# Kernel tuning notes

Measured on AMD Instinct MI355X. Metric: run time of the kernel, lower is better.

Reference implementation:

```python
import jax, jax.numpy as jnp
import numpy as np

N_HASHES = 4
CHUNK = 144
REDUCTION = 4
RES_SCALE = 1.0
NORM_EPS = 5e-5


def conv2d(x, w, b, pad):
    y = jax.lax.conv_general_dilated(
        x, w, window_strides=(1, 1), padding=[(pad, pad), (pad, pad)],
        dimension_numbers=('NCHW', 'OIHW', 'NCHW'))
    return y + b[None, :, None, None]


def add_adjacent_buckets(x):
    # x: (N, h, n_chunks, chunk, e); concat each chunk with its circular neighbors
    back = jnp.roll(x, 1, axis=2)
    fwd = jnp.roll(x, -1, axis=2)
    return jnp.concatenate([x, back, fwd], axis=3)


def setup_inputs() -> dict:
    key = jax.random.key(0)
    ks = jax.random.split(key, 6)
    x = jax.random.normal(ks[0], (1, 32, 192, 192), jnp.float32)
    w_match = jax.random.normal(ks[1], (8, 32, 3, 3), jnp.float32) * 0.05
    b_match = jnp.zeros((8,), jnp.float32)
    w_asm = jax.random.normal(ks[2], (32, 32, 1, 1), jnp.float32) * 0.05
    b_asm = jnp.zeros((32,), jnp.float32)
    rotations = jax.random.normal(ks[3], (8, N_HASHES, 64), jnp.float32)
    return {'x': x, 'w_match': w_match, 'b_match': b_match,
            'w_asm': w_asm, 'b_asm': b_asm, 'rotations': rotations}


def reference(x, w_match, b_match, w_asm, b_asm, rotations):
    N, _, H, W = x.shape
    L = H * W
    # conv_match: 3x3 conv 32->8; conv_assembly: 1x1 conv 32->32
    x_embed = conv2d(x, w_match, b_match, 1).reshape(N, -1, L).transpose(0, 2, 1)  # (N, L, 8)
    y_embed = conv2d(x, w_asm, b_asm, 0).reshape(N, -1, L).transpose(0, 2, 1)      # (N, L, 32)
    C = x_embed.shape[-1]
    hash_buckets = min(L // CHUNK + (L // CHUNK) % 2, 128)  # = 128 here

    # --- LSH hashing (non-differentiable; rotations passed in for determinism) ---
    rotated = jnp.einsum('blf,fhi->bhli', x_embed, rotations)        # (N, h, L, hb/2)
    rotated = jnp.concatenate([rotated, -rotated], axis=-1)          # (N, h, L, hb)
    hash_codes = jnp.argmax(rotated, axis=-1)                        # (N, h, L)
    hash_codes = hash_codes + (jnp.arange(N_HASHES) * hash_buckets)[None, :, None]
    hash_codes = hash_codes.reshape(N, -1)                           # (N, h*L)

    # --- sort tokens by bucket id ---
    indices = jnp.argsort(hash_codes, axis=-1)
    undo_sort = jnp.argsort(indices, axis=-1)
    mod_indices = indices % L
    x_sorted = jnp.take_along_axis(x_embed, mod_indices[:, :, None], axis=1)  # (N, h*L, 8)
    y_sorted = jnp.take_along_axis(y_embed, mod_indices[:, :, None], axis=1)  # (N, h*L, 32)

    x_b = x_sorted.reshape(N, N_HASHES, -1, C)
    y_b = y_sorted.reshape(N, N_HASHES, -1, C * REDUCTION)
    padding = (-L) % CHUNK  # static; 0 for L=192*192
    if padding:
        x_b = jnp.concatenate([x_b, x_b[:, :, -padding:, :]], axis=2)
        y_b = jnp.concatenate([y_b, y_b[:, :, -padding:, :]], axis=2)
    x_b = x_b.reshape(N, N_HASHES, -1, CHUNK, C)
    y_b = y_b.reshape(N, N_HASHES, -1, CHUNK, C * REDUCTION)

    # --- bucketed attention with adjacent buckets ---
    nrm = jnp.linalg.norm(x_b, axis=-1, keepdims=True)
    x_match = x_b / jnp.maximum(nrm, NORM_EPS)   # F.normalize(eps=5e-5)
    x_match = add_adjacent_buckets(x_match)      # (N, h, k, 3*chunk, 8)
    y_adj = add_adjacent_buckets(y_b)            # (N, h, k, 3*chunk, 32)

    raw = jnp.einsum('bhkie,bhkje->bhkij', x_b, x_match)  # (N, h, k, 144, 432)
    bucket_score = jax.scipy.special.logsumexp(raw, axis=-1, keepdims=True)
    score = jnp.exp(raw - bucket_score)
    ret = jnp.einsum('bhkij,bhkje->bhkie', score, y_adj)  # (N, h, k, 144, 32)

    ret = ret.reshape(N, N_HASHES, -1, C * REDUCTION)
    bucket_score = bucket_score.reshape(N, N_HASHES, -1)
    if padding:
        ret = ret[:, :, :-padding, :]
        bucket_score = bucket_score[:, :, :-padding]
    ret = ret.reshape(N, -1, C * REDUCTION)
    bucket_score = bucket_score.reshape(N, -1)

    # --- unsort and combine hash rounds via softmax over logsumexp scores ---
    ret = jnp.take_along_axis(ret, undo_sort[:, :, None], axis=1)
    bucket_score = jnp.take_along_axis(bucket_score, undo_sort, axis=1)
    ret = ret.reshape(N, N_HASHES, L, C * REDUCTION)
    probs = jax.nn.softmax(bucket_score.reshape(N, N_HASHES, L, 1), axis=1)
    out = jnp.sum(ret * probs, axis=1)                     # (N, L, 32)
    out = out.transpose(0, 2, 1).reshape(N, -1, H, W) * RES_SCALE + x
    return out
```

## Files before the change

### kernel.cpp

```cpp
#include <hip/hip_runtime.h>
#include <hip/hip_bf16.h>
#include <math.h>

#define LTOT 36864
#define NH 4
#define NCHUNK 256
#define CHU 144
#define NBUCK 128
#define NSEG 144
#define HW_ 192
#define VTS 148

typedef unsigned int u32;
typedef unsigned short u16;
typedef unsigned long long u64;
typedef __attribute__((ext_vector_type(4))) short short4v;
typedef __attribute__((ext_vector_type(4))) float f32x4;

__device__ __forceinline__ u32 pkbf(float a, float b){
  union { __hip_bfloat162 h2; u32 u; } cv;
  cv.h2 = __float22bfloat162_rn(float2{a,b});
  return cv.u;
}
__device__ __forceinline__ float bflo(u32 w){ return __uint_as_float(w<<16); }
__device__ __forceinline__ float bfhi(u32 w){ return __uint_as_float(w & 0xffff0000u); }

__global__ __launch_bounds__(256) void k_conv(const float* __restrict__ x,
    const float* __restrict__ wm, const float* __restrict__ bm,
    const float* __restrict__ wa, const float* __restrict__ ba,
    const float* __restrict__ rot,
    float* __restrict__ xe, u16* __restrict__ Vu, int* __restrict__ code)
{
  __shared__ float xs[32*108];
  __shared__ float xq[64*8];
  const int t = threadIdx.x;
  const int id = blockIdx.x;
  const int bx = id % 12, by = id / 12;

  for (int idx=t; idx<3456; idx+=256){
    int ci = idx/108, rem = idx-ci*108;
    int iy = rem/18,  ix = rem-iy*18;
    int yy = by*4+iy-1, xx = bx*16+ix-1;
    float v = 0.f;
    if (yy>=0 && yy<HW_ && xx>=0 && xx<HW_) v = x[ci*LTOT + yy*HW_ + xx];
    xs[idx] = v;
  }
  __syncthreads();
  const int lane = t & 63;
  const int w  = __builtin_amdgcn_readfirstlane(t>>6);
  const int co0 = 2*w, cb = 8*w;
  const int ix = lane & 15, iy = lane >> 4;
  float a0 = bm[co0], a1 = bm[co0+1];
  float acc[8];
  #pragma unroll
  for (int co=0;co<8;co++) acc[co] = ba[cb+co];
  const float* xb  = xs + iy*18 + ix;
  const float* w0p = wm + co0*288;
  const float* w1p = w0p + 288;
  for (int ci=0; ci<32; ci++){
    const float* xp = xb + ci*108;
    float x00=xp[0],  x01=xp[1],  x02=xp[2];
    float x10=xp[18], x11=xp[19], x12=xp[20];
    float x20=xp[36], x21=xp[37], x22=xp[38];
    const float* w0 = w0p + ci*9;
    const float* w1 = w1p + ci*9;
    a0 += x00*w0[0]+x01*w0[1]+x02*w0[2]
        + x10*w0[3]+x11*w0[4]+x12*w0[5]
        + x20*w0[6]+x21*w0[7]+x22*w0[8];
    a1 += x00*w1[0]+x01*w1[1]+x02*w1[2]
        + x10*w1[3]+x11*w1[4]+x12*w1[5]
        + x20*w1[6]+x21*w1[7]+x22*w1[8];
    const float* wap = wa + cb*32 + ci;
    #pragma unroll
    for (int co=0;co<8;co++) acc[co] += x11 * wap[co*32];
  }
  const int l = (by*4+iy)*HW_ + bx*16+ix;
  *(float2*)(xe + l*8 + co0) = float2{a0,a1};
  *(float2*)(xq + lane*8 + co0) = float2{a0,a1};
  uint4 vv;
  vv.x = pkbf(acc[0],acc[1]); vv.y = pkbf(acc[2],acc[3]);
  vv.z = pkbf(acc[4],acc[5]); vv.w = pkbf(acc[6],acc[7]);
  *(uint4*)(Vu + (size_t)l*32 + cb) = vv;
  __syncthreads();

  const int h = w;
  const float4* qp = (const float4*)(xq + lane*8);
  float4 qa = qp[0], qb = qp[1];
  float best = -INFINITY; int bi = 0;
  float worst = INFINITY; int wi = 0;
  for (int i=0; i<64; i++){
    const float* rp = rot + h*64 + i;
    float v = qa.x*rp[0]    + qa.y*rp[256]  + qa.z*rp[512]  + qa.w*rp[768]
            + qb.x*rp[1024] + qb.y*rp[1280] + qb.z*rp[1536] + qb.w*rp[1792];
    if (v > best)  { best  = v; bi = i; }
    if (v < worst) { worst = v; wi = i; }
  }
  int c = (-worst > best) ? (64+wi) : bi;
  const int ly = lane >> 4, lx = lane & 15;
  code[h*LTOT + (by*4+ly)*HW_ + bx*16+lx] = c;
}

__global__ __launch_bounds__(256) void k_rank(const int* __restrict__ code,
    int* __restrict__ lrank, int* __restrict__ hist)
{
  const int h = blockIdx.y, seg = blockIdx.x, t = threadIdx.x;
  const int l = seg*256 + t;
  int c = code[h*LTOT + l];

  const int lane = t & 63, w = t >> 6;
  u64 mask = ~0ull;
  #pragma unroll
  for (int bit=0; bit<7; bit++){
    u64 bset = __ballot((c>>bit)&1);
    mask &= ((c>>bit)&1) ? bset : ~bset;
  }
  int rin = __popcll(mask & ((lane==0)?0ull:(~0ull >> (64-lane))));
  int cnt = __popcll(mask);

  __shared__ int wh[4][NBUCK];
  ((int*)wh)[t] = 0; ((int*)wh)[t+256] = 0;
  __syncthreads();
  if (rin == 0) wh[w][c] = cnt;
  __syncthreads();
  int r = rin;
  for (int ww=0; ww<w; ww++) r += wh[ww][c];
  lrank[h*LTOT + l] = r;
  if (t < NBUCK) hist[(h*NSEG+seg)*NBUCK + t] = wh[0][t]+wh[1][t]+wh[2][t]+wh[3][t];
}

__global__ __launch_bounds__(512) void k_scan(const int* __restrict__ hist,
    int* __restrict__ segoff)
{
  const int h = blockIdx.x;
  const int b = threadIdx.x & 127, g = threadIdx.x >> 7;
  int vals[36];
  int sum = 0;
  #pragma unroll
  for (int i=0;i<36;i++){
    vals[i] = hist[(h*NSEG + g*36 + i)*NBUCK + b];
    sum += vals[i];
  }
  __shared__ int ps[4][NBUCK];
  __shared__ int tot[NBUCK];
  __shared__ int scv[NBUCK];
  ps[g][b] = sum;
  __syncthreads();
  if (g == 0){
    int run = 0;
    #pragma unroll
    for (int gg=0; gg<4; gg++){ int tv = ps[gg][b]; ps[gg][b] = run; run += tv; }
    tot[b] = run;
    int v = run;
    #pragma unroll
    for (int off=1; off<64; off<<=1){
      int u = __shfl_up(v, off);
      if ((b & 63) >= off) v += u;
    }
    scv[b] = v;
  }
  __syncthreads();
  int base = scv[b] - tot[b] + ((b >= 64) ? scv[63] : 0);
  int run2 = base + ps[g][b];
  #pragma unroll
  for (int i=0;i<36;i++){
    segoff[(h*NSEG + g*36 + i)*NBUCK + b] = run2;
    run2 += vals[i];
  }
}

__global__ __launch_bounds__(256) void k_scatter(const int* __restrict__ code,
    const int* __restrict__ lrank, const int* __restrict__ segoff,
    const float* __restrict__ xe, const u16* __restrict__ Vu,
    int* __restrict__ spos, u16* __restrict__ Ks, u16* __restrict__ Qs,
    u16* __restrict__ Vs)
{
  const int h = blockIdx.y, seg = blockIdx.x, t = threadIdx.x;
  const int l = seg*256 + t;
  int c = code[h*LTOT + l];
  int r = segoff[(h*NSEG+seg)*NBUCK + c] + lrank[h*LTOT + l];
  spos[h*LTOT + r] = l;

  const float4* xr = (const float4*)(xe + l*8);
  float4 a = xr[0], b = xr[1];
  float n2 = a.x*a.x+a.y*a.y+a.z*a.z+a.w*a.w
           + b.x*b.x+b.y*b.y+b.z*b.z+b.w*b.w;
  float sc = 1.0f / fmaxf(sqrtf(n2), 5e-5f);
  uint4 kk, qq;
  kk.x = pkbf(a.x*sc,a.y*sc); kk.y = pkbf(a.z*sc,a.w*sc);
  kk.z = pkbf(b.x*sc,b.y*sc); kk.w = pkbf(b.z*sc,b.w*sc);
  qq.x = pkbf(a.x,a.y); qq.y = pkbf(a.z,a.w);
  qq.z = pkbf(b.x,b.y); qq.w = pkbf(b.z,b.w);
  *(uint4*)(Ks + (size_t)(h*LTOT + r)*8) = kk;
  *(uint4*)(Qs + (size_t)(h*LTOT + r)*8) = qq;

  const uint4* vr = (const uint4*)(Vu + (size_t)l*32);
  uint4* vp = (uint4*)(Vs + (size_t)(h*LTOT + r)*32);
  vp[0] = vr[0]; vp[1] = vr[1]; vp[2] = vr[2]; vp[3] = vr[3];
}

__global__ __launch_bounds__(320) void k_attn(const u16* __restrict__ Ks,
    const u16* __restrict__ Qs, const u16* __restrict__ Vs,
    const int* __restrict__ spos, u16* __restrict__ ret_u, float* __restrict__ bs_u)
{
  __shared__ __align__(16) u16 Klds[432*8];
  __shared__ __align__(16) u16 Qlds[CHU*8];
  __shared__ __align__(16) u16 VT[3][32*VTS];
  __shared__ float qn[CHU];
  __shared__ int spos_l[CHU];

  const int t = threadIdx.x;
  const int k = blockIdx.x, h = blockIdx.y;

  if (t < CHU){
    uint4 qv = *(const uint4*)(Qs + (size_t)(h*LTOT + k*CHU + t)*8);
    *(uint4*)(Qlds + t*8) = qv;
    float f0=bflo(qv.x), f1=bfhi(qv.x), f2=bflo(qv.y), f3=bfhi(qv.y);
    float f4=bflo(qv.z), f5=bfhi(qv.z), f6=bflo(qv.w), f7=bfhi(qv.w);
    qn[t] = sqrtf(f0*f0+f1*f1+f2*f2+f3*f3+f4*f4+f5*f5+f6*f6+f7*f7)*1.01f + 1e-6f;
    spos_l[t] = spos[h*LTOT + k*CHU + t];
    #pragma unroll
    for (int rr=0; rr<3; rr++){
      const int gkb = ((k + NCHUNK-1 + rr) & (NCHUNK-1)) * CHU;
      *(uint4*)(Klds + (rr*CHU + t)*8) =
          *(const uint4*)(Ks + (size_t)(h*LTOT + gkb + t)*8);
    }
  }
  for (int j = t; j < 432; j += 320){
    int p = j >> 1, hf = j & 1;
    int g = 2*p;
    int rg = g / CHU, lk = g - rg*CHU;
    const int gkb = ((k + NCHUNK-1 + rg) & (NCHUNK-1)) * CHU;
    const uint4* ra = (const uint4*)(Vs + (size_t)(h*LTOT + gkb + lk)*32);
    const uint4* rb = (const uint4*)(Vs + (size_t)(h*LTOT + gkb + lk+1)*32);
    uint4 A0 = ra[hf*2], A1 = ra[hf*2+1];
    uint4 B0 = rb[hf*2], B1 = rb[hf*2+1];
    u32 aw[8] = {A0.x,A0.y,A0.z,A0.w,A1.x,A1.y,A1.z,A1.w};
    u32 bw[8] = {B0.x,B0.y,B0.z,B0.w,B1.x,B1.y,B1.z,B1.w};
    int ebase = hf*16;
    u16* vtb = (u16*)VT[rg];
    #pragma unroll
    for (int m=0;m<8;m++){
      u32 al = aw[m]&0xffffu, ah = aw[m]>>16;
      u32 bl = bw[m]&0xffffu, bh = bw[m]>>16;
      *(u32*)&vtb[(ebase+2*m  )*VTS + lk] = al | (bl<<16);
      *(u32*)&vtb[(ebase+2*m+1)*VTS + lk] = ah | (bh<<16);
    }
  }
  __syncthreads();

  const int lane = t & 63;
  const int wv = t >> 6;
  const int q = lane & 15;
  const int quad = lane >> 4;
  const bool two = (wv < 4);
  const int tl0 = 2*wv;
  const int tl1 = two ? (2*wv+1) : 8;

  const short4v zs = {0,0,0,0};
  short4v bq0 = zs, bq1 = zs;
  if (quad < 2){
    bq0 = *(const short4v*)(Qlds + (tl0*16+q)*8 + quad*4);
    if (two) bq1 = *(const short4v*)(Qlds + (tl1*16+q)*8 + quad*4);
  }
  const float m0 = qn[tl0*16+q];
  const float m1 = two ? qn[tl1*16+q] : 0.f;

  f32x4 o00={0,0,0,0}, o01={0,0,0,0}, o10={0,0,0,0}, o11={0,0,0,0};
  float s0 = 0.f, s1 = 0.f;

  #pragma unroll 3
  for (int kt=0; kt<27; kt++){
    const int rg = kt / 9, ktl = kt - rg*9;
    const u16* vtb = VT[rg];
    short4v av = zs;
    if (quad < 2) av = *(const short4v*)(Klds + (kt*16+q)*8 + quad*4);
    f32x4 zc = {0.f,0.f,0.f,0.f};
    f32x4 stA = __builtin_amdgcn_mfma_f32_16x16x16bf16_1k(av, bq0, zc, 0,0,0);

    float pA0 = __expf(stA[0]-m0), pA1 = __expf(stA[1]-m0);
    float pA2 = __expf(stA[2]-m0), pA3 = __expf(stA[3]-m0);
    s0 += (pA0+pA1)+(pA2+pA3);
    union { u32 u[2]; short4v s4; } pkA;
    pkA.u[0] = pkbf(pA0,pA1); pkA.u[1] = pkbf(pA2,pA3);

    short4v va0 = *(const short4v*)(&vtb[ q    *VTS + ktl*16 + quad*4]);
    short4v va1 = *(const short4v*)(&vtb[(q+16)*VTS + ktl*16 + quad*4]);
    o00 = __builtin_amdgcn_mfma_f32_16x16x16bf16_1k(va0, pkA.s4, o00, 0,0,0);
    o01 = __builtin_amdgcn_mfma_f32_16x16x16bf16_1k(va1, pkA.s4, o01, 0,0,0);

    if (two){
      f32x4 stB = __builtin_amdgcn_mfma_f32_16x16x16bf16_1k(av, bq1, zc, 0,0,0);
      float pB0 = __expf(stB[0]-m1), pB1 = __expf(stB[1]-m1);
      float pB2 = __expf(stB[2]-m1), pB3 = __expf(stB[3]-m1);
      s1 += (pB0+pB1)+(pB2+pB3);
      union { u32 u[2]; short4v s4; } pkB;
      pkB.u[0] = pkbf(pB0,pB1); pkB.u[1] = pkbf(pB2,pB3);
      o10 = __builtin_amdgcn_mfma_f32_16x16x16bf16_1k(va0, pkB.s4, o10, 0,0,0);
      o11 = __builtin_amdgcn_mfma_f32_16x16x16bf16_1k(va1, pkB.s4, o11, 0,0,0);
    }
  }

  float st0 = s0;
  st0 += __shfl_xor(st0, 16); st0 += __shfl_xor(st0, 32);
  float inv0 = 1.0f/st0;

  const int pos0 = spos_l[tl0*16 + q];
  u16* rp0 = ret_u + (size_t)(h*LTOT + pos0)*32;
  uint2 wA, wB;
  wA.x = pkbf(o00[0]*inv0, o00[1]*inv0); wA.y = pkbf(o00[2]*inv0, o00[3]*inv0);
  wB.x = pkbf(o01[0]*inv0, o01[1]*inv0); wB.y = pkbf(o01[2]*inv0, o01[3]*inv0);
  *(uint2*)&rp0[quad*4]    = wA;
  *(uint2*)&rp0[16+quad*4] = wB;
  if (quad == 0) bs_u[h*LTOT + pos0] = m0 + __logf(st0);

  if (two){
    float st1 = s1;
    st1 += __shfl_xor(st1, 16); st1 += __shfl_xor(st1, 32);
    float inv1 = 1.0f/st1;
    const int pos1 = spos_l[tl1*16 + q];
    u16* rp1 = ret_u + (size_t)(h*LTOT + pos1)*32;
    wA.x = pkbf(o10[0]*inv1, o10[1]*inv1); wA.y = pkbf(o10[2]*inv1, o10[3]*inv1);
    wB.x = pkbf(o11[0]*inv1, o11[1]*inv1); wB.y = pkbf(o11[2]*inv1, o11[3]*inv1);
    *(uint2*)&rp1[quad*4]    = wA;
    *(uint2*)&rp1[16+quad*4] = wB;
    if (quad == 0) bs_u[h*LTOT + pos1] = m1 + __logf(st1);
  }
}

__global__ __launch_bounds__(256) void k_final(const float* __restrict__ x,
    const u16* __restrict__ ret_u, const float* __restrict__ bs_u,
    float* __restrict__ out)
{
  const int l  = blockIdx.x*64 + (threadIdx.x & 63);
  const int eg = threadIdx.x >> 6;
  float bs[NH];
  #pragma unroll
  for (int h=0;h<NH;h++) bs[h] = bs_u[h*LTOT + l];
  float m = fmaxf(fmaxf(bs[0],bs[1]), fmaxf(bs[2],bs[3]));
  float p[NH]; float s = 0.f;
  #pragma unroll
  for (int h=0;h<NH;h++){ p[h] = __expf(bs[h]-m); s += p[h]; }
  float inv = 1.0f/s;
  float o[8];
  #pragma unroll
  for (int e=0;e<8;e++) o[e]=0.f;
  #pragma unroll
  for (int h=0;h<NH;h++){
    float w = p[h]*inv;
    uint4 v = *(const uint4*)(ret_u + (size_t)(h*LTOT + l)*32 + eg*8);
    o[0] += w*bflo(v.x); o[1] += w*bfhi(v.x);
    o[2] += w*bflo(v.y); o[3] += w*bfhi(v.y);
    o[4] += w*bflo(v.z); o[5] += w*bfhi(v.z);
    o[6] += w*bflo(v.w); o[7] += w*bfhi(v.w);
  }
  #pragma unroll
  for (int e=0;e<8;e++){
    int ge = eg*8 + e;
    out[ge*LTOT + l] = o[e] + x[ge*LTOT + l];
  }
}

extern "C" void kernel_launch(void* const* d_in, const int* in_sizes, int n_in,
                              void* d_out, int out_size, void* d_ws, size_t ws_size,
                              hipStream_t stream)
{
  const float* x   = (const float*)d_in[0];
  const float* wm  = (const float*)d_in[1];
  const float* bm  = (const float*)d_in[2];
  const float* wa  = (const float*)d_in[3];
  const float* ba  = (const float*)d_in[4];
  const float* rot = (const float*)d_in[5];
  float* out = (float*)d_out;

  char* ws = (char*)d_ws;
  size_t off = 0;
  auto alloc = [&](size_t bytes)->void*{
    void* p = ws + off;
    off = (off + bytes + 255) & ~(size_t)255;
    return p;
  };
  float* xe     = (float*)alloc((size_t)LTOT*8*4);
  u16*   Vu     = (u16*)  alloc((size_t)LTOT*32*2);
  int*   code   = (int*)  alloc((size_t)NH*LTOT*4);
  int*   lrank  = (int*)  alloc((size_t)NH*LTOT*4);
  int*   hist   = (int*)  alloc((size_t)NH*NSEG*NBUCK*4);
  int*   segoff = (int*)  alloc((size_t)NH*NSEG*NBUCK*4);
  int*   spos   = (int*)  alloc((size_t)NH*LTOT*4);
  u16*   Ks     = (u16*)  alloc((size_t)NH*LTOT*8*2);
  u16*   Qs     = (u16*)  alloc((size_t)NH*LTOT*8*2);
  u16*   Vs     = (u16*)  alloc((size_t)NH*LTOT*32*2);
  u16*   ret_u  = (u16*)  alloc((size_t)NH*LTOT*32*2);
  float* bs_u   = (float*)alloc((size_t)NH*LTOT*4);

  hipLaunchKernelGGL(k_conv,    dim3(576),        dim3(256), 0, stream, x, wm, bm, wa, ba, rot, xe, Vu, code);
  hipLaunchKernelGGL(k_rank,    dim3(NSEG,NH),    dim3(256), 0, stream, code, lrank, hist);
  hipLaunchKernelGGL(k_scan,    dim3(NH),         dim3(512), 0, stream, hist, segoff);
  hipLaunchKernelGGL(k_scatter, dim3(NSEG,NH),    dim3(256), 0, stream, code, lrank, segoff, xe, Vu, spos, Ks, Qs, Vs);
  hipLaunchKernelGGL(k_attn,    dim3(NCHUNK,NH),  dim3(320), 0, stream, Ks, Qs, Vs, spos, ret_u, bs_u);
  hipLaunchKernelGGL(k_final,   dim3(576),        dim3(256), 0, stream, x, ret_u, bs_u, out);
}
```

Before: 130.3 us.

## Fuse histogram into conv and rank/scan into scatter, dropping two launches

The conv kernel now runs 512 threads per block, with one match channel and four assembly channels per wave instead of two and eight. It also builds the per-segment bucket histogram with global atomics after hashing. The separate rank and scan kernels are gone: each scatter block recomputes its intra-segment rank with ballots and its global offset by summing the histogram over all segments. This removes two launches and the lrank/segoff buffers, but adds a memset, atomics, and redundant prefix reads of 144 segments in every scatter block.

```diff
diff --git a/kernel.cpp b/kernel.cpp
--- a/kernel.cpp
+++ b/kernel.cpp
@@ -25,11 +25,12 @@
 __device__ __forceinline__ float bflo(u32 w){ return __uint_as_float(w<<16); }
 __device__ __forceinline__ float bfhi(u32 w){ return __uint_as_float(w & 0xffff0000u); }
 
-__global__ __launch_bounds__(256) void k_conv(const float* __restrict__ x,
+__global__ __launch_bounds__(512) void k_conv(const float* __restrict__ x,
     const float* __restrict__ wm, const float* __restrict__ bm,
     const float* __restrict__ wa, const float* __restrict__ ba,
     const float* __restrict__ rot,
-    float* __restrict__ xe, u16* __restrict__ Vu, int* __restrict__ code)
+    float* __restrict__ xe, u16* __restrict__ Vu, int* __restrict__ code,
+    int* __restrict__ hist)
 {
   __shared__ float xs[32*108];
   __shared__ float xq[64*8];
@@ -37,7 +38,7 @@
   const int id = blockIdx.x;
   const int bx = id % 12, by = id / 12;
 
-  for (int idx=t; idx<3456; idx+=256){
+  for (int idx=t; idx<3456; idx+=512){
     int ci = idx/108, rem = idx-ci*108;
     int iy = rem/18,  ix = rem-iy*18;
     int yy = by*4+iy-1, xx = bx*16+ix-1;
@@ -48,65 +49,83 @@
   __syncthreads();
   const int lane = t & 63;
   const int w  = __builtin_amdgcn_readfirstlane(t>>6);
-  const int co0 = 2*w, cb = 8*w;
+  const int co = w;
+  const int cb = 4*w;
   const int ix = lane & 15, iy = lane >> 4;
-  float a0 = bm[co0], a1 = bm[co0+1];
-  float acc[8];
-  #pragma unroll
-  for (int co=0;co<8;co++) acc[co] = ba[cb+co];
+  float a0 = bm[co];
+  float acc[4];
+  #pragma unroll
+  for (int j=0;j<4;j++) acc[j] = ba[cb+j];
   const float* xb  = xs + iy*18 + ix;
-  const float* w0p = wm + co0*288;
-  const float* w1p = w0p + 288;
+  const float* w0p = wm + co*288;
   for (int ci=0; ci<32; ci++){
     const float* xp = xb + ci*108;
     float x00=xp[0],  x01=xp[1],  x02=xp[2];
     float x10=xp[18], x11=xp[19], x12=xp[20];
     float x20=xp[36], x21=xp[37], x22=xp[38];
     const float* w0 = w0p + ci*9;
-    const float* w1 = w1p + ci*9;
     a0 += x00*w0[0]+x01*w0[1]+x02*w0[2]
         + x10*w0[3]+x11*w0[4]+x12*w0[5]
         + x20*w0[6]+x21*w0[7]+x22*w0[8];
-    a1 += x00*w1[0]+x01*w1[1]+x02*w1[2]
-        + x10*w1[3]+x11*w1[4]+x12*w1[5]
-        + x20*w1[6]+x21*w1[7]+x22*w1[8];
     const float* wap = wa + cb*32 + ci;
     #pragma unroll
-    for (int co=0;co<8;co++) acc[co] += x11 * wap[co*32];
+    for (int j=0;j<4;j++) acc[j] += x11 * wap[j*32];
   }
   const int l = (by*4+iy)*HW_ + bx*16+ix;
-  *(float2*)(xe + l*8 + co0) = float2{a0,a1};
-  *(float2*)(xq + lane*8 + co0) = float2{a0,a1};
-  uint4 vv;
+  xe[l*8 + co] = a0;
+  xq[lane*8 + co] = a0;
+  uint2 vv;
   vv.x = pkbf(acc[0],acc[1]); vv.y = pkbf(acc[2],acc[3]);
-  vv.z = pkbf(acc[4],acc[5]); vv.w = pkbf(acc[6],acc[7]);
-  *(uint4*)(Vu + (size_t)l*32 + cb) = vv;
-  __syncthreads();
-
-  const int h = w;
-  const float4* qp = (const float4*)(xq + lane*8);
-  float4 qa = qp[0], qb = qp[1];
-  float best = -INFINITY; int bi = 0;
-  float worst = INFINITY; int wi = 0;
-  for (int i=0; i<64; i++){
-    const float* rp = rot + h*64 + i;
-    float v = qa.x*rp[0]    + qa.y*rp[256]  + qa.z*rp[512]  + qa.w*rp[768]
-            + qb.x*rp[1024] + qb.y*rp[1280] + qb.z*rp[1536] + qb.w*rp[1792];
-    if (v > best)  { best  = v; bi = i; }
-    if (v < worst) { worst = v; wi = i; }
-  }
-  int c = (-worst > best) ? (64+wi) : bi;
-  const int ly = lane >> 4, lx = lane & 15;
-  code[h*LTOT + (by*4+ly)*HW_ + bx*16+lx] = c;
-}
-
-__global__ __launch_bounds__(256) void k_rank(const int* __restrict__ code,
-    int* __restrict__ lrank, int* __restrict__ hist)
+  *(uint2*)(Vu + (size_t)l*32 + cb) = vv;
+  __syncthreads();
+
+  if (t < 256){
+    const int h = w;
+    const float4* qp = (const float4*)(xq + lane*8);
+    float4 qa = qp[0], qb = qp[1];
+    float best = -INFINITY; int bi = 0;
+    float worst = INFINITY; int wi = 0;
+    for (int i=0; i<64; i++){
+      const float* rp = rot + h*64 + i;
+      float v = qa.x*rp[0]    + qa.y*rp[256]  + qa.z*rp[512]  + qa.w*rp[768]
+              + qb.x*rp[1024] + qb.y*rp[1280] + qb.z*rp[1536] + qb.w*rp[1792];
+      if (v > best)  { best  = v; bi = i; }
+      if (v < worst) { worst = v; wi = i; }
+    }
+    int c = (-worst > best) ? (64+wi) : bi;
+    const int ly = lane >> 4, lx = lane & 15;
+    const int lpix = (by*4+ly)*HW_ + bx*16+lx;
+    code[h*LTOT + lpix] = c;
+    atomicAdd(&hist[(h*NSEG + (lpix>>8))*NBUCK + c], 1);
+  }
+}
+
+__global__ __launch_bounds__(256) void k_scatter(const int* __restrict__ code,
+    const int* __restrict__ hist,
+    const float* __restrict__ xe, const u16* __restrict__ Vu,
+    int* __restrict__ spos, u16* __restrict__ Ks, u16* __restrict__ Qs,
+    u16* __restrict__ Vs)
 {
   const int h = blockIdx.y, seg = blockIdx.x, t = threadIdx.x;
   const int l = seg*256 + t;
   int c = code[h*LTOT + l];
 
+  __shared__ int pre2[2][NBUCK], tot2[2][NBUCK];
+  __shared__ int scv[NBUCK];
+  __shared__ int segbase[NBUCK];
+  __shared__ int wh[4][NBUCK];
+
+  {
+    const int b = t & 127, gg = t >> 7;
+    int pre = 0, tt = 0;
+    const int sA = gg*72;
+    for (int s = sA; s < sA+72; s++){
+      int v = hist[(h*NSEG+s)*NBUCK + b];
+      tt += v;
+      if (s < seg) pre += v;
+    }
+    pre2[gg][b] = pre; tot2[gg][b] = tt;
+  }
   const int lane = t & 63, w = t >> 6;
   u64 mask = ~0ull;
   #pragma unroll
@@ -116,68 +135,31 @@
   }
   int rin = __popcll(mask & ((lane==0)?0ull:(~0ull >> (64-lane))));
   int cnt = __popcll(mask);
-
-  __shared__ int wh[4][NBUCK];
   ((int*)wh)[t] = 0; ((int*)wh)[t+256] = 0;
   __syncthreads();
+
   if (rin == 0) wh[w][c] = cnt;
-  __syncthreads();
-  int r = rin;
-  for (int ww=0; ww<w; ww++) r += wh[ww][c];
-  lrank[h*LTOT + l] = r;
-  if (t < NBUCK) hist[(h*NSEG+seg)*NBUCK + t] = wh[0][t]+wh[1][t]+wh[2][t]+wh[3][t];
-}
-
-__global__ __launch_bounds__(512) void k_scan(const int* __restrict__ hist,
-    int* __restrict__ segoff)
-{
-  const int h = blockIdx.x;
-  const int b = threadIdx.x & 127, g = threadIdx.x >> 7;
-  int vals[36];
-  int sum = 0;
-  #pragma unroll
-  for (int i=0;i<36;i++){
-    vals[i] = hist[(h*NSEG + g*36 + i)*NBUCK + b];
-    sum += vals[i];
-  }
-  __shared__ int ps[4][NBUCK];
-  __shared__ int tot[NBUCK];
-  __shared__ int scv[NBUCK];
-  ps[g][b] = sum;
-  __syncthreads();
-  if (g == 0){
-    int run = 0;
-    #pragma unroll
-    for (int gg=0; gg<4; gg++){ int tv = ps[gg][b]; ps[gg][b] = run; run += tv; }
-    tot[b] = run;
-    int v = run;
+  if (t < NBUCK){
+    int tt = tot2[0][t] + tot2[1][t];
+    int v = tt;
     #pragma unroll
     for (int off=1; off<64; off<<=1){
       int u = __shfl_up(v, off);
-      if ((b & 63) >= off) v += u;
-    }
-    scv[b] = v;
-  }
-  __syncthreads();
-  int base = scv[b] - tot[b] + ((b >= 64) ? scv[63] : 0);
-  int run2 = base + ps[g][b];
-  #pragma unroll
-  for (int i=0;i<36;i++){
-    segoff[(h*NSEG + g*36 + i)*NBUCK + b] = run2;
-    run2 += vals[i];
-  }
-}
-
-__global__ __launch_bounds__(256) void k_scatter(const int* __restrict__ code,
-    const int* __restrict__ lrank, const int* __restrict__ segoff,
-    const float* __restrict__ xe, const u16* __restrict__ Vu,
-    int* __restrict__ spos, u16* __restrict__ Ks, u16* __restrict__ Qs,
-    u16* __restrict__ Vs)
-{
-  const int h = blockIdx.y, seg = blockIdx.x, t = threadIdx.x;
-  const int l = seg*256 + t;
-  int c = code[h*LTOT + l];
-  int r = segoff[(h*NSEG+seg)*NBUCK + c] + lrank[h*LTOT + l];
+      if ((t & 63) >= off) v += u;
+    }
+    scv[t] = v;
+  }
+  __syncthreads();
+
+  if (t < NBUCK){
+    int tt = tot2[0][t] + tot2[1][t];
+    int excl = scv[t] - tt + ((t >= 64) ? scv[63] : 0);
+    segbase[t] = excl + pre2[0][t] + pre2[1][t];
+  }
+  __syncthreads();
+
+  int r = segbase[c] + rin;
+  for (int ww=0; ww<w; ww++) r += wh[ww][c];
   spos[h*LTOT + r] = l;
 
   const float4* xr = (const float4*)(xe + l*8);
@@ -382,9 +364,7 @@
   float* xe     = (float*)alloc((size_t)LTOT*8*4);
   u16*   Vu     = (u16*)  alloc((size_t)LTOT*32*2);
   int*   code   = (int*)  alloc((size_t)NH*LTOT*4);
-  int*   lrank  = (int*)  alloc((size_t)NH*LTOT*4);
   int*   hist   = (int*)  alloc((size_t)NH*NSEG*NBUCK*4);
-  int*   segoff = (int*)  alloc((size_t)NH*NSEG*NBUCK*4);
   int*   spos   = (int*)  alloc((size_t)NH*LTOT*4);
   u16*   Ks     = (u16*)  alloc((size_t)NH*LTOT*8*2);
   u16*   Qs     = (u16*)  alloc((size_t)NH*LTOT*8*2);
@@ -392,10 +372,9 @@
   u16*   ret_u  = (u16*)  alloc((size_t)NH*LTOT*32*2);
   float* bs_u   = (float*)alloc((size_t)NH*LTOT*4);
 
-  hipLaunchKernelGGL(k_conv,    dim3(576),        dim3(256), 0, stream, x, wm, bm, wa, ba, rot, xe, Vu, code);
-  hipLaunchKernelGGL(k_rank,    dim3(NSEG,NH),    dim3(256), 0, stream, code, lrank, hist);
-  hipLaunchKernelGGL(k_scan,    dim3(NH),         dim3(512), 0, stream, hist, segoff);
-  hipLaunchKernelGGL(k_scatter, dim3(NSEG,NH),    dim3(256), 0, stream, code, lrank, segoff, xe, Vu, spos, Ks, Qs, Vs);
+  hipMemsetAsync(hist, 0, (size_t)NH*NSEG*NBUCK*4, stream);
+  hipLaunchKernelGGL(k_conv,    dim3(576),        dim3(512), 0, stream, x, wm, bm, wa, ba, rot, xe, Vu, code, hist);
+  hipLaunchKernelGGL(k_scatter, dim3(NSEG,NH),    dim3(256), 0, stream, code, hist, xe, Vu, spos, Ks, Qs, Vs);
   hipLaunchKernelGGL(k_attn,    dim3(NCHUNK,NH),  dim3(320), 0, stream, Ks, Qs, Vs, spos, ret_u, bs_u);
   hipLaunchKernelGGL(k_final,   dim3(576),        dim3(256), 0, stream, x, ret_u, bs_u, out);
 }
```

Result: slower. 134.4 us (+3.2%).
